# Optimization experiments

Measured on AMD Instinct MI355X. Metric: run time of the kernel, lower is better.

## Reference

```python
import jax, jax.numpy as jnp
import numpy as np

IN_FEATURES = 4096
OUT_FEATURES = 4096
BLOCK_SIZE = 16
E2M1_VALUES = jnp.array([0.0, 0.5, 1.0, 1.5, 2.0, 3.0, 4.0, 6.0], dtype=jnp.float32)


def dequantize_nvfp4(weight_packed, weight_scales, out_features, in_features, block_size, dtype):
    # Unpack two 4-bit codes per byte: even positions = high nibble, odd = low nibble
    p = weight_packed.astype(jnp.int32)
    high = (p >> 4) & 15
    low = p & 15
    unpacked = jnp.stack([high, low], axis=-1).reshape(-1)  # [out*in]
    sign = ((unpacked >> 3) & 1).astype(dtype)
    mag_code = unpacked & 7
    magnitude = E2M1_VALUES.astype(dtype)[mag_code]
    vals = jnp.where(sign == 1, -magnitude, magnitude)
    # Expand per-block E4M3 scales (repeat_interleave)
    scales_expanded = jnp.repeat(weight_scales.astype(dtype), block_size)
    w = vals * scales_expanded
    return w.reshape(out_features, in_features)


def setup_inputs() -> dict:
    key = jax.random.key(0)
    k1, k2, k3, k4 = jax.random.split(key, 4)
    x = jax.random.normal(k1, (4, 2048, IN_FEATURES), dtype=jnp.float32)
    weight_packed = jax.random.randint(k2, (OUT_FEATURES * IN_FEATURES // 2,), 0, 256, dtype=jnp.int32)
    weight_scales = jax.random.uniform(k3, (OUT_FEATURES * IN_FEATURES // BLOCK_SIZE,), dtype=jnp.float32)
    bias = jax.random.normal(k4, (OUT_FEATURES,), dtype=jnp.float32)
    return {"x": x, "weight_packed": weight_packed, "weight_scales": weight_scales, "bias": bias}


def reference(x, weight_packed, weight_scales, bias):
    w = dequantize_nvfp4(weight_packed, weight_scales, OUT_FEATURES, IN_FEATURES, BLOCK_SIZE, x.dtype)
    # F.linear: y = x @ w.T + bias
    return jnp.einsum('bsi,oi->bso', x, w) + bias
```

## Files before the change

### kernel.cpp

```cpp
#include <hip/hip_runtime.h>
#include <cstdint>
#include <cstddef>

#define MDIM 8192
#define NDIM 4096
#define KDIM 4096

typedef __attribute__((ext_vector_type(8))) __bf16 bf16x8;
typedef __attribute__((ext_vector_type(4))) float floatx4;

typedef __attribute__((address_space(3))) void lds_t;
typedef __attribute__((address_space(1))) void glb_t;

__device__ __forceinline__ unsigned short f32_to_bf16(float f) {
  unsigned int u = __float_as_uint(f);
  u += 0x7FFFu + ((u >> 16) & 1u);
  return (unsigned short)(u >> 16);
}

__device__ __forceinline__ float fp4_mag(int c) {
  int e = (c >> 1) & 3, m = c & 1;
  int sh = e ? (e - 1) : 0;
  return e ? 0.5f * (float)((2 + m) << sh) : 0.5f * (float)m;
}

__global__ __launch_bounds__(256) void conv_x_kernel(const float* __restrict__ x,
                                                     unsigned short* __restrict__ xb) {
  const int t = blockIdx.x * 256 + threadIdx.x;
  const float4* src = (const float4*)x + (size_t)t * 2;
  float4 a = src[0], b = src[1];
  union { unsigned short us[8]; uint4 u4; } o;
  o.us[0] = f32_to_bf16(a.x); o.us[1] = f32_to_bf16(a.y);
  o.us[2] = f32_to_bf16(a.z); o.us[3] = f32_to_bf16(a.w);
  o.us[4] = f32_to_bf16(b.x); o.us[5] = f32_to_bf16(b.y);
  o.us[6] = f32_to_bf16(b.z); o.us[7] = f32_to_bf16(b.w);
  ((uint4*)xb)[t] = o.u4;
}

__global__ __launch_bounds__(256) void dequant_kernel(const int* __restrict__ packed,
                                                      const float* __restrict__ scales,
                                                      unsigned short* __restrict__ wb) {
  const int t = blockIdx.x * 256 + threadIdx.x;
  const int4* p = (const int4*)packed + (size_t)t * 2;
  int4 pa = p[0], pb = p[1];
  float s = scales[t];
  int bytes[8] = {pa.x, pa.y, pa.z, pa.w, pb.x, pb.y, pb.z, pb.w};
  union { unsigned short us[16]; uint4 u4[2]; } o;
#pragma unroll
  for (int i = 0; i < 8; ++i) {
    int by = bytes[i] & 255;
    int hi = by >> 4, lo = by & 15;
    float vh = fp4_mag(hi & 7) * s; if (hi & 8) vh = -vh;
    float vl = fp4_mag(lo & 7) * s; if (lo & 8) vl = -vl;
    o.us[2 * i]     = f32_to_bf16(vh);
    o.us[2 * i + 1] = f32_to_bf16(vl);
  }
  uint4* dst = (uint4*)(wb + (size_t)t * 16);
  dst[0] = o.u4[0]; dst[1] = o.u4[1];
}

__global__ __launch_bounds__(256, 3) void gemm_kernel(const __bf16* __restrict__ A,
                                                      const __bf16* __restrict__ B,
                                                      const float* __restrict__ bias,
                                                      float* __restrict__ C) {
  __shared__ __bf16 As[128 * 32];
  __shared__ __bf16 Bs[128 * 32];
  const int t = threadIdx.x;
  const int wave = t >> 6, lane = t & 63;
  const int quad = lane >> 4, r16 = lane & 15;
  const int wm = (wave >> 1) * 64, wn = (wave & 1) * 64;
  const int m0 = blockIdx.y * 128, n0 = blockIdx.x * 128;

  floatx4 acc[4][4] = {};

  const int sr = t >> 2;
  const int sc = (t & 3) * 8;

  const __bf16* ga = A + (size_t)(m0 + sr) * KDIM + sc;
  const __bf16* gb = B + (size_t)(n0 + sr) * KDIM + sc;

  for (int k0 = 0; k0 < KDIM; k0 += 32) {
    __builtin_amdgcn_global_load_lds((const glb_t*)(ga),
                                     (lds_t*)(As + wave * 512), 16, 0, 0);
    __builtin_amdgcn_global_load_lds((const glb_t*)(ga + (size_t)64 * KDIM),
                                     (lds_t*)(As + 2048 + wave * 512), 16, 0, 0);
    __builtin_amdgcn_global_load_lds((const glb_t*)(gb),
                                     (lds_t*)(Bs + wave * 512), 16, 0, 0);
    __builtin_amdgcn_global_load_lds((const glb_t*)(gb + (size_t)64 * KDIM),
                                     (lds_t*)(Bs + 2048 + wave * 512), 16, 0, 0);
    ga += 32; gb += 32;
    __syncthreads();

    bf16x8 af[4], bfr[4];
#pragma unroll
    for (int i = 0; i < 4; ++i) {
      af[i]  = *(const bf16x8*)(As + (wm + i * 16 + r16) * 32 + quad * 8);
      bfr[i] = *(const bf16x8*)(Bs + (wn + i * 16 + r16) * 32 + quad * 8);
    }
#pragma unroll
    for (int i = 0; i < 4; ++i)
#pragma unroll
      for (int j = 0; j < 4; ++j)
        acc[i][j] = __builtin_amdgcn_mfma_f32_16x16x32_bf16(af[i], bfr[j], acc[i][j], 0, 0, 0);
    __syncthreads();
  }

  float bv[4];
#pragma unroll
  for (int j = 0; j < 4; ++j) bv[j] = bias[n0 + wn + j * 16 + r16];
#pragma unroll
  for (int i = 0; i < 4; ++i) {
    const int gm = m0 + wm + i * 16 + quad * 4;
#pragma unroll
    for (int j = 0; j < 4; ++j) {
      float* cp = C + (size_t)gm * NDIM + (n0 + wn + j * 16 + r16);
#pragma unroll
      for (int r = 0; r < 4; ++r)
        cp[(size_t)r * NDIM] = acc[i][j][r] + bv[j];
    }
  }
}

__global__ __launch_bounds__(256) void fused_fallback(const float* __restrict__ x,
                                                      const int* __restrict__ packed,
                                                      const float* __restrict__ scales,
                                                      const float* __restrict__ bias,
                                                      float* __restrict__ out) {
  const int n = blockIdx.x * 256 + threadIdx.x;
  const int m = blockIdx.y;
  const float* xr = x + (size_t)m * KDIM;
  const int* pr = packed + (size_t)n * (KDIM / 2);
  const float* sc = scales + (size_t)n * (KDIM / 16);
  float acc = 0.f;
  for (int kb = 0; kb < KDIM / 16; ++kb) {
    float s = sc[kb];
    float part = 0.f;
#pragma unroll
    for (int i = 0; i < 8; ++i) {
      int by = pr[kb * 8 + i] & 255;
      int hi = by >> 4, lo = by & 15;
      float vh = fp4_mag(hi & 7); if (hi & 8) vh = -vh;
      float vl = fp4_mag(lo & 7); if (lo & 8) vl = -vl;
      part += xr[kb * 16 + 2 * i] * vh + xr[kb * 16 + 2 * i + 1] * vl;
    }
    acc += s * part;
  }
  out[(size_t)m * NDIM + n] = acc + bias[n];
}

extern "C" void kernel_launch(void* const* d_in, const int* in_sizes, int n_in,
                              void* d_out, int out_size, void* d_ws, size_t ws_size,
                              hipStream_t stream) {
  const float* x      = (const float*)d_in[0];
  const int*   packed = (const int*)d_in[1];
  const float* scales = (const float*)d_in[2];
  const float* bias   = (const float*)d_in[3];
  float* out = (float*)d_out;

  const size_t needA = (size_t)MDIM * KDIM * 2;
  const size_t needW = (size_t)NDIM * KDIM * 2;

  if (ws_size >= needA + needW) {
    unsigned short* xb = (unsigned short*)d_ws;
    unsigned short* wb = (unsigned short*)((char*)d_ws + needA);
    conv_x_kernel<<<(MDIM * KDIM / 8) / 256, 256, 0, stream>>>(x, xb);
    dequant_kernel<<<(NDIM * KDIM / 16) / 256, 256, 0, stream>>>(packed, scales, wb);
    dim3 grid(NDIM / 128, MDIM / 128);
    gemm_kernel<<<grid, 256, 0, stream>>>((const __bf16*)xb, (const __bf16*)wb, bias, out);
  } else {
    dim3 grid(NDIM / 256, MDIM);
    fused_fallback<<<grid, 256, 0, stream>>>(x, packed, scales, bias, out);
  }
}
```

Measured before the change: 561.4 us.

## Rewrite GEMM as 256x256 tile with 4-stage LDS pipeline and swizzle

Replaces the 128x128 single-buffered GEMM with a 512-thread 256x256 tile kernel. It uses a 4-deep LDS ring fed by async global-to-LDS loads with manual vmcnt waits, an XOR swizzle to avoid LDS bank conflicts, a remapped block order for L2 locality, and setprio around the MFMA bursts. The goal is to hide global load latency and raise operand reuse per block. In exchange it uses 128KB of LDS, which allows only one block per CU, and it depends on hand-counted wait counts that must match the number of loads in flight.

```diff
diff --git a/kernel.cpp b/kernel.cpp
--- a/kernel.cpp
+++ b/kernel.cpp
@@ -59,61 +59,102 @@
   dst[0] = o.u4[0]; dst[1] = o.u4[1];
 }
 
-__global__ __launch_bounds__(256, 3) void gemm_kernel(const __bf16* __restrict__ A,
+__global__ __launch_bounds__(512) void gemm256_kernel(const __bf16* __restrict__ A,
                                                       const __bf16* __restrict__ B,
                                                       const float* __restrict__ bias,
                                                       float* __restrict__ C) {
-  __shared__ __bf16 As[128 * 32];
-  __shared__ __bf16 Bs[128 * 32];
+  __shared__ __bf16 ldsbuf[65536];
+  __bf16* As = ldsbuf;
+  __bf16* Bs = ldsbuf + 32768;
+
   const int t = threadIdx.x;
   const int wave = t >> 6, lane = t & 63;
   const int quad = lane >> 4, r16 = lane & 15;
-  const int wm = (wave >> 1) * 64, wn = (wave & 1) * 64;
-  const int m0 = blockIdx.y * 128, n0 = blockIdx.x * 128;
-
-  floatx4 acc[4][4] = {};
-
-  const int sr = t >> 2;
-  const int sc = (t & 3) * 8;
-
-  const __bf16* ga = A + (size_t)(m0 + sr) * KDIM + sc;
-  const __bf16* gb = B + (size_t)(n0 + sr) * KDIM + sc;
-
-  for (int k0 = 0; k0 < KDIM; k0 += 32) {
-    __builtin_amdgcn_global_load_lds((const glb_t*)(ga),
-                                     (lds_t*)(As + wave * 512), 16, 0, 0);
-    __builtin_amdgcn_global_load_lds((const glb_t*)(ga + (size_t)64 * KDIM),
-                                     (lds_t*)(As + 2048 + wave * 512), 16, 0, 0);
-    __builtin_amdgcn_global_load_lds((const glb_t*)(gb),
-                                     (lds_t*)(Bs + wave * 512), 16, 0, 0);
-    __builtin_amdgcn_global_load_lds((const glb_t*)(gb + (size_t)64 * KDIM),
-                                     (lds_t*)(Bs + 2048 + wave * 512), 16, 0, 0);
-    ga += 32; gb += 32;
-    __syncthreads();
-
-    bf16x8 af[4], bfr[4];
-#pragma unroll
-    for (int i = 0; i < 4; ++i) {
-      af[i]  = *(const bf16x8*)(As + (wm + i * 16 + r16) * 32 + quad * 8);
-      bfr[i] = *(const bf16x8*)(Bs + (wn + i * 16 + r16) * 32 + quad * 8);
-    }
-#pragma unroll
-    for (int i = 0; i < 4; ++i)
-#pragma unroll
-      for (int j = 0; j < 4; ++j)
-        acc[i][j] = __builtin_amdgcn_mfma_f32_16x16x32_bf16(af[i], bfr[j], acc[i][j], 0, 0, 0);
-    __syncthreads();
-  }
+  const int wr = wave >> 2, wc = wave & 3;
+
+  const int bid = blockIdx.x;
+  const int wg = (bid & 7) * 64 + (bid >> 3);
+  const int m0 = (wg >> 4) * 256, n0 = (wg & 15) * 256;
+
+  const int swzS = ((t >> 3) & 7) << 4;
+  const int b0 = (t * 16) ^ swzS;
+  const int b1 = (8192 + t * 16) ^ swzS;
+  const int row0 = b0 >> 6, col0 = (b0 & 63) >> 1;
+  const int row1 = b1 >> 6, col1 = (b1 & 63) >> 1;
+
+  const __bf16* pa0 = A + (size_t)(m0 + row0) * KDIM + col0;
+  const __bf16* pa1 = A + (size_t)(m0 + row1) * KDIM + col1;
+  const __bf16* pb0 = B + (size_t)(n0 + row0) * KDIM + col0;
+  const __bf16* pb1 = B + (size_t)(n0 + row1) * KDIM + col1;
+
+  const int swzR = ((r16 >> 1) & 7) << 4;
+  const int offAe = ((((wr * 128 + r16) * 64) + quad * 16) ^ swzR) >> 1;
+  const int offBe = ((((wc * 64  + r16) * 64) + quad * 16) ^ swzR) >> 1;
+
+  floatx4 acc[8][4] = {};
+
+#define STAGE(TT) do {                                                                              \
+    const int _kk = (TT) * 32;                                                                      \
+    __bf16* _ab = As + ((TT) & 3) * 8192;                                                           \
+    __bf16* _bb = Bs + ((TT) & 3) * 8192;                                                           \
+    __builtin_amdgcn_global_load_lds((const glb_t*)(pa0 + _kk), (lds_t*)(_ab + wave * 512), 16, 0, 0);        \
+    __builtin_amdgcn_global_load_lds((const glb_t*)(pa1 + _kk), (lds_t*)(_ab + 4096 + wave * 512), 16, 0, 0); \
+    __builtin_amdgcn_global_load_lds((const glb_t*)(pb0 + _kk), (lds_t*)(_bb + wave * 512), 16, 0, 0);        \
+    __builtin_amdgcn_global_load_lds((const glb_t*)(pb1 + _kk), (lds_t*)(_bb + 4096 + wave * 512), 16, 0, 0); \
+  } while (0)
+
+#define BARRIER() asm volatile("s_barrier" ::: "memory")
+
+#define COMPUTE(TT) do {                                                          \
+    const __bf16* _a = As + ((TT) & 3) * 8192;                                    \
+    const __bf16* _b = Bs + ((TT) & 3) * 8192;                                    \
+    bf16x8 af[8], bfv[4];                                                         \
+    _Pragma("unroll")                                                             \
+    for (int i = 0; i < 8; ++i) af[i] = *(const bf16x8*)(_a + offAe + i * 512);   \
+    _Pragma("unroll")                                                             \
+    for (int j = 0; j < 4; ++j) bfv[j] = *(const bf16x8*)(_b + offBe + j * 512);  \
+    __builtin_amdgcn_s_setprio(1);                                                \
+    _Pragma("unroll")                                                             \
+    for (int i = 0; i < 8; ++i) {                                                 \
+      _Pragma("unroll")                                                           \
+      for (int j = 0; j < 4; ++j)                                                 \
+        acc[i][j] = __builtin_amdgcn_mfma_f32_16x16x32_bf16(af[i], bfv[j], acc[i][j], 0, 0, 0); \
+    }                                                                             \
+    __builtin_amdgcn_s_setprio(0);                                                \
+    BARRIER();                                                                    \
+  } while (0)
+
+  STAGE(0); STAGE(1); STAGE(2);
+
+  for (int T = 0; T < 125; ++T) {
+    STAGE(T + 3);
+    asm volatile("s_waitcnt vmcnt(12)" ::: "memory");
+    BARRIER();
+    COMPUTE(T);
+  }
+  asm volatile("s_waitcnt vmcnt(8)" ::: "memory");
+  BARRIER();
+  COMPUTE(125);
+  asm volatile("s_waitcnt vmcnt(4)" ::: "memory");
+  BARRIER();
+  COMPUTE(126);
+  asm volatile("s_waitcnt vmcnt(0)" ::: "memory");
+  BARRIER();
+  COMPUTE(127);
+
+#undef STAGE
+#undef BARRIER
+#undef COMPUTE
 
   float bv[4];
 #pragma unroll
-  for (int j = 0; j < 4; ++j) bv[j] = bias[n0 + wn + j * 16 + r16];
-#pragma unroll
-  for (int i = 0; i < 4; ++i) {
-    const int gm = m0 + wm + i * 16 + quad * 4;
+  for (int j = 0; j < 4; ++j) bv[j] = bias[n0 + wc * 64 + j * 16 + r16];
+#pragma unroll
+  for (int i = 0; i < 8; ++i) {
+    const int gm = m0 + wr * 128 + i * 16 + quad * 4;
 #pragma unroll
     for (int j = 0; j < 4; ++j) {
-      float* cp = C + (size_t)gm * NDIM + (n0 + wn + j * 16 + r16);
+      float* cp = C + (size_t)gm * NDIM + (n0 + wc * 64 + j * 16 + r16);
 #pragma unroll
       for (int r = 0; r < 4; ++r)
         cp[(size_t)r * NDIM] = acc[i][j][r] + bv[j];
@@ -165,8 +206,8 @@
     unsigned short* wb = (unsigned short*)((char*)d_ws + needA);
     conv_x_kernel<<<(MDIM * KDIM / 8) / 256, 256, 0, stream>>>(x, xb);
     dequant_kernel<<<(NDIM * KDIM / 16) / 256, 256, 0, stream>>>(packed, scales, wb);
-    dim3 grid(NDIM / 128, MDIM / 128);
-    gemm_kernel<<<grid, 256, 0, stream>>>((const __bf16*)xb, (const __bf16*)wb, bias, out);
+    dim3 grid((MDIM / 256) * (NDIM / 256));
+    gemm256_kernel<<<grid, 512, 0, stream>>>((const __bf16*)xb, (const __bf16*)wb, bias, out);
   } else {
     dim3 grid(NDIM / 256, MDIM);
     fused_fallback<<<grid, 256, 0, stream>>>(x, packed, scales, bias, out);
```

Measured after the change: 502.7 us. 1.12x faster.
